# Kernel tuning notes

Measured on AMD Instinct MI355X. Metric: run time of the kernel, lower is better.

Reference implementation:

```python
import jax, jax.numpy as jnp
import numpy as np

B, N = 4, 4096
CIN, COUT = 64, 64
K, R, BOX = 3, 32, 4
MLP = COUT * 4
HEADS = 4
EPS = 0.0


def setup_inputs() -> dict:
    key = jax.random.key(0)
    ks = jax.random.split(key, 16)
    s = lambda i, shape: jax.random.normal(ks[i], shape, jnp.float32) * 0.05
    return dict(
        features=jax.random.normal(ks[0], (B, CIN, N), jnp.float32),
        coords=jax.random.normal(ks[1], (B, 3, N), jnp.float32),
        conv_w=s(2, (COUT, CIN, K, K, K)), conv_b=jnp.zeros((COUT,), jnp.float32),
        ln1_g=jnp.ones((COUT,), jnp.float32), ln1_b=jnp.zeros((COUT,), jnp.float32),
        qkv_w=s(3, (3 * COUT, COUT)), qkv_b=jnp.zeros((3 * COUT,), jnp.float32),
        proj_w=s(4, (COUT, COUT)), proj_b=jnp.zeros((COUT,), jnp.float32),
        ln2_g=jnp.ones((COUT,), jnp.float32), ln2_b=jnp.zeros((COUT,), jnp.float32),
        mlp_w1=s(5, (MLP, COUT)), mlp_b1=jnp.zeros((MLP,), jnp.float32),
        mlp_w2=s(6, (COUT, MLP)), mlp_b2=jnp.zeros((COUT,), jnp.float32),
        se_w1=s(7, (COUT // 8, COUT)), se_w2=s(8, (COUT, COUT // 8)),
        pt_in_w=s(9, (COUT, CIN)), pt_in_b=jnp.zeros((COUT,), jnp.float32),
        q_w=s(10, (COUT // 4, COUT)), k_w=s(11, (COUT // 4, COUT)),
        v_w=s(12, (COUT, COUT)),
        trans_w=s(13, (COUT, COUT)), trans_b=jnp.zeros((COUT,), jnp.float32),
    )


def layernorm(x, g, b):
    m = x.mean(-1, keepdims=True)
    v = x.var(-1, keepdims=True)
    return (x - m) * jax.lax.rsqrt(v + 1e-5) * g + b


def voxelize(features, coords):
    # PVCNN-style: center, normalize to [0,1], scale to [0, R-1]; scatter-mean.
    c = coords - coords.mean(axis=2, keepdims=True)  # (B,3,N)
    mx = jnp.sqrt((c ** 2).sum(axis=1, keepdims=True)).max(axis=2, keepdims=True)
    nc = c / (2.0 * mx + EPS) + 0.5
    nc = jnp.clip(nc * R, 0.0, R - 1)  # float coords in [0, R-1]
    vc = jnp.round(nc).astype(jnp.int32)
    idx = (vc[:, 0] * R + vc[:, 1]) * R + vc[:, 2]
    idx = (idx + jnp.arange(B, dtype=jnp.int32)[:, None] * R ** 3).reshape(-1)
    flat = features.transpose(0, 2, 1).reshape(B * N, CIN)
    sums = jax.ops.segment_sum(flat, idx, num_segments=B * R ** 3)
    cnt = jax.ops.segment_sum(jnp.ones((B * N,), jnp.float32), idx, num_segments=B * R ** 3)
    avg = sums / jnp.maximum(cnt, 1.0)[:, None]
    grid = avg.reshape(B, R, R, R, CIN).transpose(0, 4, 1, 2, 3)  # (B,C,R,R,R)
    return grid, nc


def devoxelize(grid, nc):
    # trilinear gather from (B,C,R,R,R) at float coords nc (B,3,N)
    g = grid.reshape(B, COUT, R ** 3)
    x0 = jnp.floor(nc)
    f = nc - x0
    x0 = x0.astype(jnp.int32)
    out = jnp.zeros((B, COUT, N), jnp.float32)
    for dx in (0, 1):
        for dy in (0, 1):
            for dz in (0, 1):
                xi = jnp.clip(x0[:, 0] + dx, 0, R - 1)
                yi = jnp.clip(x0[:, 1] + dy, 0, R - 1)
                zi = jnp.clip(x0[:, 2] + dz, 0, R - 1)
                idx = (xi * R + yi) * R + zi  # (B,N)
                w = ((f[:, 0] if dx else 1 - f[:, 0]) *
                     (f[:, 1] if dy else 1 - f[:, 1]) *
                     (f[:, 2] if dz else 1 - f[:, 2]))
                vals = jnp.take_along_axis(g, jnp.broadcast_to(idx[:, None, :], (B, COUT, N)), axis=2)
                out = out + vals * w[:, None, :]
    return out


def voxel_encoder(grid, conv_w, conv_b, ln1_g, ln1_b, qkv_w, qkv_b, proj_w, proj_b,
                  ln2_g, ln2_b, mlp_w1, mlp_b1, mlp_w2, mlp_b2):
    x = jax.lax.conv_general_dilated(grid, conv_w, (1, 1, 1), 'SAME',
                                     dimension_numbers=('NCDHW', 'OIDHW', 'NCDHW'))
    x = jax.nn.relu(x + conv_b[None, :, None, None, None])
    nb = R // BOX
    # window partition -> (B*nb^3, BOX^3, C)
    t = x.transpose(0, 2, 3, 4, 1).reshape(B, nb, BOX, nb, BOX, nb, BOX, COUT)
    t = t.transpose(0, 1, 3, 5, 2, 4, 6, 7).reshape(B * nb ** 3, BOX ** 3, COUT)
    h = layernorm(t, ln1_g, ln1_b)
    qkv = h @ qkv_w.T + qkv_b
    q, k, v = jnp.split(qkv, 3, axis=-1)
    hd = COUT // HEADS
    sh = lambda z: z.reshape(z.shape[0], z.shape[1], HEADS, hd).transpose(0, 2, 1, 3)
    q, k, v = sh(q), sh(k), sh(v)
    attn = jax.nn.softmax(jnp.einsum('whid,whjd->whij', q, k) / np.float32(np.sqrt(hd)), axis=-1)
    o = jnp.einsum('whij,whjd->whid', attn, v).transpose(0, 2, 1, 3).reshape(t.shape)
    t = t + (o @ proj_w.T + proj_b)
    h = layernorm(t, ln2_g, ln2_b)
    t = t + (jax.nn.gelu(h @ mlp_w1.T + mlp_b1) @ mlp_w2.T + mlp_b2)
    t = t.reshape(B, nb, nb, nb, BOX, BOX, BOX, COUT)
    t = t.transpose(0, 1, 4, 2, 5, 3, 6, 7).reshape(B, R, R, R, COUT)
    return t.transpose(0, 4, 1, 2, 3)


def se3d(x, w1, w2):
    s = x.mean(axis=(2, 3, 4))  # (B,C)
    s = jax.nn.sigmoid(jax.nn.relu(s @ w1.T) @ w2.T)
    return x * s[:, :, None, None, None]


def point_branch(features, pt_in_w, pt_in_b, q_w, k_w, v_w, trans_w, trans_b):
    # PCT-style offset self-attention over points (shared transformer)
    x = jax.nn.relu(jnp.einsum('oc,bcn->bon', pt_in_w, features) + pt_in_b[None, :, None])
    q = jnp.einsum('dc,bcn->bdn', q_w, x)
    k = jnp.einsum('dc,bcn->bdn', k_w, x)
    v = jnp.einsum('oc,bcn->bon', v_w, x)
    attn = jax.nn.softmax(jnp.einsum('bdn,bdm->bnm', q, k) / np.float32(np.sqrt(q.shape[1])), axis=-1)
    o = jnp.einsum('bom,bnm->bon', v, attn)
    off = jax.nn.relu(jnp.einsum('oc,bcn->bon', trans_w, x - o) + trans_b[None, :, None])
    return x + off


def reference(features, coords, conv_w, conv_b, ln1_g, ln1_b, qkv_w, qkv_b, proj_w, proj_b,
              ln2_g, ln2_b, mlp_w1, mlp_b1, mlp_w2, mlp_b2, se_w1, se_w2,
              pt_in_w, pt_in_b, q_w, k_w, v_w, trans_w, trans_b):
    grid, nc = voxelize(features, coords)
    vf = voxel_encoder(grid, conv_w, conv_b, ln1_g, ln1_b, qkv_w, qkv_b, proj_w, proj_b,
                       ln2_g, ln2_b, mlp_w1, mlp_b1, mlp_w2, mlp_b2)
    vf = se3d(vf, se_w1, se_w2)
    vf = devoxelize(vf, nc)
    fused = vf + point_branch(features, pt_in_w, pt_in_b, q_w, k_w, v_w, trans_w, trans_b)
    return fused, coords
```

## Files before the change

### kernel.cpp

```cpp
#include <hip/hip_runtime.h>

#define BN 4
#define NP 4096
#define RV 32
#define VX (RV*RV*RV)

typedef __attribute__((ext_vector_type(8))) short bf16x8;
typedef __attribute__((ext_vector_type(4))) float f32x4;

__device__ __forceinline__ float bf2f(unsigned short u){
  union{unsigned u;float f;}v; v.u=((unsigned)u)<<16; return v.f; }
__device__ __forceinline__ unsigned short f2bf(float f){
  union{float f;unsigned u;}v; v.f=f; unsigned r=v.u + 0x7fffu + ((v.u>>16)&1u);
  return (unsigned short)(r>>16); }
__device__ __forceinline__ float2 bfp2f2(unsigned p){
  union{unsigned u;float f;}a,b; a.u=p<<16; b.u=p&0xffff0000u;
  float2 r; r.x=a.f; r.y=b.f; return r; }
__device__ __forceinline__ unsigned pack2bf(float a, float b){
  return (unsigned)f2bf(a) | ((unsigned)f2bf(b) << 16); }

union ABu { uint4 u; bf16x8 v; };

__global__ void stats_kernel(const float* __restrict__ coords, float* __restrict__ stats)
{
  __shared__ float red[256];
  __shared__ float mean[3];
  const int b = blockIdx.x;
  const int tid = threadIdx.x;
  float s0=0.f,s1=0.f,s2=0.f;
  for (int n = tid; n < NP; n += 256) {
    s0 += coords[((size_t)(b*3)+0)*NP + n];
    s1 += coords[((size_t)(b*3)+1)*NP + n];
    s2 += coords[((size_t)(b*3)+2)*NP + n];
  }
  float sv[3] = {s0,s1,s2};
  for (int ax = 0; ax < 3; ax++) {
    __syncthreads();
    red[tid] = sv[ax];
    __syncthreads();
    for (int st = 128; st > 0; st >>= 1) {
      if (tid < st) red[tid] += red[tid + st];
      __syncthreads();
    }
    if (tid == 0) mean[ax] = red[0] * (1.f / NP);
  }
  __syncthreads();
  float mx = 0.f;
  for (int n = tid; n < NP; n += 256) {
    float d0 = coords[((size_t)(b*3)+0)*NP + n] - mean[0];
    float d1 = coords[((size_t)(b*3)+1)*NP + n] - mean[1];
    float d2 = coords[((size_t)(b*3)+2)*NP + n] - mean[2];
    mx = fmaxf(mx, sqrtf(d0*d0 + d1*d1 + d2*d2));
  }
  __syncthreads();
  red[tid] = mx;
  __syncthreads();
  for (int st = 128; st > 0; st >>= 1) {
    if (tid < st) red[tid] = fmaxf(red[tid], red[tid + st]);
    __syncthreads();
  }
  if (tid == 0) {
    stats[b*4+0] = mean[0]; stats[b*4+1] = mean[1];
    stats[b*4+2] = mean[2]; stats[b*4+3] = red[0];
  }
}

__global__ void scatter_kernel(const float* __restrict__ features,
                               const float* __restrict__ coords,
                               const float* __restrict__ stats,
                               float* __restrict__ nc,
                               float* __restrict__ sums, float* __restrict__ cnt)
{
  int t = blockIdx.x*256 + threadIdx.x;
  int part = t & 3;
  int p = t >> 2;
  int b = p >> 12;
  int n = p & 4095;
  float m0 = stats[b*4+0], m1 = stats[b*4+1], m2 = stats[b*4+2], mx = stats[b*4+3];
  float inv = 1.f / (2.f * mx);
  float c0 = (coords[((size_t)(b*3)+0)*NP + n] - m0) * inv + 0.5f;
  float c1 = (coords[((size_t)(b*3)+1)*NP + n] - m1) * inv + 0.5f;
  float c2 = (coords[((size_t)(b*3)+2)*NP + n] - m2) * inv + 0.5f;
  float g0 = fminf(fmaxf(c0 * 32.f, 0.f), 31.f);
  float g1 = fminf(fmaxf(c1 * 32.f, 0.f), 31.f);
  float g2 = fminf(fmaxf(c2 * 32.f, 0.f), 31.f);
  int v0 = (int)rintf(g0), v1 = (int)rintf(g1), v2 = (int)rintf(g2);
  int idx = (v0*32 + v1)*32 + v2 + b*VX;
  if (part == 0) {
    nc[((size_t)(b*3)+0)*NP + n] = g0;
    nc[((size_t)(b*3)+1)*NP + n] = g1;
    nc[((size_t)(b*3)+2)*NP + n] = g2;
    atomicAdd(&cnt[idx], 1.f);
  }
  const float* fp = features + (size_t)(b*64)*NP + n;
  float* sp = sums + (size_t)idx*64;
  for (int i = part*16; i < part*16+16; i++)
    atomicAdd(&sp[i], fp[(size_t)i*NP]);
}

__global__ void wprep_kernel(const float* __restrict__ wt, unsigned short* __restrict__ wpre)
{
  int t = blockIdx.x*256 + threadIdx.x;
  if (t >= 27*64*8) return;
  int c16 = t & 7, o = (t >> 3) & 63, tap = t >> 9;
  size_t dst = ((size_t)(tap*64 + o)*8 + (c16 ^ (o & 7))) * 8;
  #pragma unroll
  for (int j = 0; j < 8; j++) {
    int i = c16*8 + j;
    wpre[dst + j] = f2bf(wt[(o*64 + i)*27 + tap]);
  }
}

__global__ void eprep_kernel(const float* __restrict__ qkv_w, const float* __restrict__ proj_w,
                             const float* __restrict__ w1, const float* __restrict__ w2,
                             unsigned short* __restrict__ dst)
{
  int t = blockIdx.x*256 + threadIdx.x;
  float v;
  if (t < 12288)      v = qkv_w[t];
  else if (t < 16384) v = proj_w[t-12288];
  else if (t < 32768) v = w1[t-16384];
  else                v = w2[t-32768];
  dst[t] = f2bf(v);
}

__global__ __launch_bounds__(256) void conv_mfma_kernel(
    const float* __restrict__ sums, const float* __restrict__ cnt,
    const unsigned short* __restrict__ wpre,
    const float* __restrict__ bias, unsigned short* __restrict__ gout)
{
  __shared__ uint4 plane[6*34*8];
  __shared__ uint4 wsm[3*64*8];
  const int tid = threadIdx.x;
  const int blk = blockIdx.x;
  const int yq = blk & 7, z = (blk >> 3) & 31, b = blk >> 8;
  const int y0 = yq * 4;
  const int w  = tid >> 6;
  const int lm = tid & 15;
  const int kg = (tid >> 4) & 3;

  f32x4 acc[2][4];
  #pragma unroll
  for (int mt = 0; mt < 2; mt++)
    #pragma unroll
    for (int nt = 0; nt < 4; nt++)
      #pragma unroll
      for (int r = 0; r < 4; r++) acc[mt][nt][r] = 0.f;

  float bv[4];
  #pragma unroll
  for (int nt = 0; nt < 4; nt++) bv[nt] = bias[nt*16 + lm];

  for (int kd = 0; kd < 3; kd++) {
    const int zz = z + kd - 1;
    if (zz < 0 || zz >= 32) continue;
    __syncthreads();
    for (int e = tid; e < 6*34*8; e += 256) {
      int c16 = e & 7;
      int sx  = (e >> 3) % 34;
      int yl  = e / (34*8);
      int yy = y0 - 1 + yl, x = sx - 1;
      uint4 val = make_uint4(0u,0u,0u,0u);
      if (yy >= 0 && yy < 32 && x >= 0 && x < 32) {
        size_t vox = (size_t)(b*VX) + (zz*32 + yy)*32 + x;
        float rc = 1.f / fmaxf(cnt[vox], 1.f);
        const float* src = sums + vox*64 + c16*8;
        float4 f0 = *(const float4*)(src);
        float4 f1 = *(const float4*)(src + 4);
        val.x = pack2bf(f0.x*rc, f0.y*rc);
        val.y = pack2bf(f0.z*rc, f0.w*rc);
        val.z = pack2bf(f1.x*rc, f1.y*rc);
        val.w = pack2bf(f1.z*rc, f1.w*rc);
      }
      plane[(yl*34 + sx)*8 + (c16 ^ (sx & 7))] = val;
    }
    for (int kh = 0; kh < 3; kh++) {
      __syncthreads();
      const uint4* wsrc = (const uint4*)wpre + (size_t)((kd*3 + kh)*3)*512;
      for (int e = tid; e < 1536; e += 256) wsm[e] = wsrc[e];
      __syncthreads();
      const int yi = w + kh;
      #pragma unroll
      for (int kw = 0; kw < 3; kw++) {
        const int sxa = lm + kw, sxb = sxa + 16;
        const int swz = sxa & 7;
        #pragma unroll
        for (int ch = 0; ch < 2; ch++) {
          const int cb = ch*4 + kg;
          ABu a0, a1, w0, w1, w2, w3;
          a0.u = plane[(yi*34 + sxa)*8 + (cb ^ swz)];
          a1.u = plane[(yi*34 + sxb)*8 + (cb ^ swz)];
          const int wsz = cb ^ (lm & 7);
          w0.u = wsm[(kw*64 +      lm)*8 + wsz];
          w1.u = wsm[(kw*64 + 16 + lm)*8 + wsz];
          w2.u = wsm[(kw*64 + 32 + lm)*8 + wsz];
          w3.u = wsm[(kw*64 + 48 + lm)*8 + wsz];
          acc[0][0] = __builtin_amdgcn_mfma_f32_16x16x32_bf16(a0.v, w0.v, acc[0][0], 0,0,0);
          acc[1][0] = __builtin_amdgcn_mfma_f32_16x16x32_bf16(a1.v, w0.v, acc[1][0], 0,0,0);
          acc[0][1] = __builtin_amdgcn_mfma_f32_16x16x32_bf16(a0.v, w1.v, acc[0][1], 0,0,0);
          acc[1][1] = __builtin_amdgcn_mfma_f32_16x16x32_bf16(a1.v, w1.v, acc[1][1], 0,0,0);
          acc[0][2] = __builtin_amdgcn_mfma_f32_16x16x32_bf16(a0.v, w2.v, acc[0][2], 0,0,0);
          acc[1][2] = __builtin_amdgcn_mfma_f32_16x16x32_bf16(a1.v, w2.v, acc[1][2], 0,0,0);
          acc[0][3] = __builtin_amdgcn_mfma_f32_16x16x32_bf16(a0.v, w3.v, acc[0][3], 0,0,0);
          acc[1][3] = __builtin_amdgcn_mfma_f32_16x16x32_bf16(a1.v, w3.v, acc[1][3], 0,0,0);
        }
      }
    }
  }
  const int y = y0 + w;
  #pragma unroll
  for (int mt = 0; mt < 2; mt++) {
    #pragma unroll
    for (int r = 0; r < 4; r++) {
      const int x = mt*16 + kg*4 + r;
      unsigned short* dst = gout + ((size_t)(b*VX) + (z*32 + y)*32 + x)*64 + lm;
      #pragma unroll
      for (int nt = 0; nt < 4; nt++)
        dst[nt*16] = f2bf(fmaxf(acc[mt][nt][r] + bv[nt], 0.f));
    }
  }
}

__global__ __launch_bounds__(256) void encoder_kernel(
    unsigned short* __restrict__ grid,
    const float* __restrict__ ln1_g, const float* __restrict__ ln1_b,
    const float* __restrict__ qkv_b, const float* __restrict__ proj_b,
    const float* __restrict__ ln2_g, const float* __restrict__ ln2_b,
    const float* __restrict__ b1, const float* __restrict__ b2,
    const unsigned short* __restrict__ encw,
    float* __restrict__ se_sum)
{
  __shared__ unsigned short t_b[64*72];
  __shared__ unsigned short h_b[64*72];
  __shared__ unsigned short q_b[64*72];
  __shared__ unsigned short k_b[64*72];
  __shared__ unsigned short v_b[64*72];
  __shared__ float mean_s[64], rstd_s[64];
  __shared__ float sered[256];

  const unsigned short* wqb = encw;
  const unsigned short* wpb = encw + 12288;
  const unsigned short* w1b = encw + 16384;
  const unsigned short* w2b = encw + 32768;

  const int tid = threadIdx.x;
  const int w = tid >> 6;
  const int lane = tid & 63;
  const int cl = lane & 15;
  const int quad = lane >> 4;
  const int win = blockIdx.x;
  const int b = win >> 9, wn = win & 511;
  const int zb = wn >> 6, yb = (wn >> 3) & 7, xb = wn & 7;
  const size_t gb = (size_t)b * VX * 64;

  for (int e = tid; e < 1024; e += 256) {
    int tok = e >> 4, cg = e & 15;
    int zl = tok >> 4, yl = (tok >> 2) & 3, xl = tok & 3;
    int vox = ((zb*4+zl)*32 + (yb*4+yl))*32 + (xb*4+xl);
    *(uint2*)(t_b + tok*72 + cg*4) = *(const uint2*)(grid + gb + (size_t)vox*64 + cg*4);
  }
  __syncthreads();
  {
    int i = tid >> 2, part = tid & 3;
    float sum = 0.f, sq = 0.f;
    for (int c = part; c < 64; c += 4) { float x = bf2f(t_b[i*72+c]); sum += x; sq += x*x; }
    sum += __shfl_xor(sum, 1); sq += __shfl_xor(sq, 1);
    sum += __shfl_xor(sum, 2); sq += __shfl_xor(sq, 2);
    if (part == 0) {
      float m = sum * (1.f/64.f);
      float var = sq * (1.f/64.f) - m*m;
      mean_s[i] = m; rstd_s[i] = rsqrtf(var + 1e-5f);
    }
  }
  __syncthreads();
  for (int e = tid; e < 4096; e += 256) {
    int tok = e >> 6, c = e & 63;
    float h = (bf2f(t_b[tok*72+c]) - mean_s[tok]) * rstd_s[tok] * ln1_g[c] + ln1_b[c];
    h_b[tok*72 + c] = f2bf(h);
  }
  __syncthreads();
  {
    #pragma unroll
    for (int ci = 0; ci < 3; ci++) {
      const int d0 = 48*w + ci*16;
      ABu a0, a1;
      a0.u = *(const uint4*)(wqb + (d0 + cl)*64 + quad*8);
      a1.u = *(const uint4*)(wqb + (d0 + cl)*64 + 32 + quad*8);
      float4 bias4 = *(const float4*)(qkv_b + d0 + quad*4);
      #pragma unroll
      for (int tt = 0; tt < 4; tt++) {
        ABu h0, h1;
        h0.u = *(const uint4*)(h_b + (tt*16 + cl)*72 + quad*8);
        h1.u = *(const uint4*)(h_b + (tt*16 + cl)*72 + 32 + quad*8);
        f32x4 d = {0.f,0.f,0.f,0.f};
        d = __builtin_amdgcn_mfma_f32_16x16x32_bf16(a0.v, h0.v, d, 0,0,0);
        d = __builtin_amdgcn_mfma_f32_16x16x32_bf16(a1.v, h1.v, d, 0,0,0);
        if (d0 < 64) {
          *(uint2*)(q_b + (tt*16+cl)*72 + d0 + quad*4) =
            make_uint2(pack2bf((d[0]+bias4.x)*0.25f, (d[1]+bias4.y)*0.25f),
                       pack2bf((d[2]+bias4.z)*0.25f, (d[3]+bias4.w)*0.25f));
        } else if (d0 < 128) {
          *(uint2*)(k_b + (tt*16+cl)*72 + (d0-64) + quad*4) =
            make_uint2(pack2bf(d[0]+bias4.x, d[1]+bias4.y),
                       pack2bf(d[2]+bias4.z, d[3]+bias4.w));
        } else {
          const float* bp = (const float*)&bias4;
          #pragma unroll
          for (int r = 0; r < 4; r++)
            v_b[((d0-128) + quad*4 + r)*72 + tt*16 + cl] = f2bf(d[r] + bp[r]);
        }
      }
    }
  }
  __syncthreads();
  uint2 pk[4];
  {
    const uint4 z4 = make_uint4(0u,0u,0u,0u);
    #pragma unroll
    for (int h = 0; h < 4; h++) {
      const int hb = h*16;
      ABu bq;
      if (quad < 2) bq.u = *(const uint4*)(q_b + (w*16 + cl)*72 + hb + quad*8);
      else bq.u = z4;
      float sc[4][4];
      #pragma unroll
      for (int tj = 0; tj < 4; tj++) {
        ABu ak;
        if (quad < 2) ak.u = *(const uint4*)(k_b + (tj*16 + cl)*72 + hb + quad*8);
        else ak.u = z4;
        f32x4 d = {0.f,0.f,0.f,0.f};
        d = __builtin_amdgcn_mfma_f32_16x16x32_bf16(ak.v, bq.v, d, 0,0,0);
        #pragma unroll
        for (int r = 0; r < 4; r++) sc[tj][r] = d[r];
      }
      float mx = -1e30f;
      #pragma unroll
      for (int tj = 0; tj < 4; tj++)
        #pragma unroll
        for (int r = 0; r < 4; r++) mx = fmaxf(mx, sc[tj][r]);
      mx = fmaxf(mx, __shfl_xor(mx, 16));
      mx = fmaxf(mx, __shfl_xor(mx, 32));
      float psum = 0.f;
      #pragma unroll
      for (int tj = 0; tj < 4; tj++) {
        float p0 = __expf(sc[tj][0]-mx), p1 = __expf(sc[tj][1]-mx);
        float p2 = __expf(sc[tj][2]-mx), p3 = __expf(sc[tj][3]-mx);
        psum += p0+p1+p2+p3;
        *(uint2*)(h_b + (w*16+cl)*72 + tj*16 + quad*4) =
            make_uint2(pack2bf(p0,p1), pack2bf(p2,p3));
      }
      psum += __shfl_xor(psum, 16);
      psum += __shfl_xor(psum, 32);
      float inv = 1.f / psum;
      f32x4 oacc = {0.f,0.f,0.f,0.f};
      #pragma unroll
      for (int kk = 0; kk < 2; kk++) {
        ABu av, bp;
        av.u = *(const uint4*)(v_b + (hb + cl)*72 + kk*32 + quad*8);
        bp.u = *(const uint4*)(h_b + (w*16 + cl)*72 + kk*32 + quad*8);
        oacc = __builtin_amdgcn_mfma_f32_16x16x32_bf16(av.v, bp.v, oacc, 0,0,0);
      }
      pk[h] = make_uint2(pack2bf(oacc[0]*inv, oacc[1]*inv),
                         pack2bf(oacc[2]*inv, oacc[3]*inv));
    }
  }
  __syncthreads();
  #pragma unroll
  for (int h = 0; h < 4; h++)
    *(uint2*)(k_b + (w*16+cl)*72 + h*16 + quad*4) = pk[h];
  __syncthreads();
  {
    const int c0 = w*16;
    ABu a0, a1;
    a0.u = *(const uint4*)(wpb + (c0 + cl)*64 + quad*8);
    a1.u = *(const uint4*)(wpb + (c0 + cl)*64 + 32 + quad*8);
    float4 pb4 = *(const float4*)(proj_b + c0 + quad*4);
    #pragma unroll
    for (int tt = 0; tt < 4; tt++) {
      ABu o0, o1;
      o0.u = *(const uint4*)(k_b + (tt*16 + cl)*72 + quad*8);
      o1.u = *(const uint4*)(k_b + (tt*16 + cl)*72 + 32 + quad*8);
      f32x4 d = {0.f,0.f,0.f,0.f};
      d = __builtin_amdgcn_mfma_f32_16x16x32_bf16(a0.v, o0.v, d, 0,0,0);
      d = __builtin_amdgcn_mfma_f32_16x16x32_bf16(a1.v, o1.v, d, 0,0,0);
      uint2* tp = (uint2*)(t_b + (tt*16+cl)*72 + c0 + quad*4);
      uint2 told = *tp;
      float2 t01 = bfp2f2(told.x), t23 = bfp2f2(told.y);
      *tp = make_uint2(pack2bf(t01.x + d[0] + pb4.x, t01.y + d[1] + pb4.y),
                       pack2bf(t23.x + d[2] + pb4.z, t23.y + d[3] + pb4.w));
    }
  }
  __syncthreads();
  {
    int i = tid >> 2, part = tid & 3;
    float sum = 0.f, sq = 0.f;
    for (int c = part; c < 64; c += 4) { float x = bf2f(t_b[i*72+c]); sum += x; sq += x*x; }
    sum += __shfl_xor(sum, 1); sq += __shfl_xor(sq, 1);
    sum += __shfl_xor(sum, 2); sq += __shfl_xor(sq, 2);
    if (part == 0) {
      float m = sum * (1.f/64.f);
      float var = sq * (1.f/64.f) - m*m;
      mean_s[i] = m; rstd_s[i] = rsqrtf(var + 1e-5f);
    }
  }
  __syncthreads();
  for (int e = tid; e < 4096; e += 256) {
    int tok = e >> 6, c = e & 63;
    float h = (bf2f(t_b[tok*72+c]) - mean_s[tok]) * rstd_s[tok] * ln2_g[c] + ln2_b[c];
    h_b[tok*72 + c] = f2bf(h);
  }
  __syncthreads();
  {
    const int c0 = w*16;
    ABu hb0[4], hb1[4];
    #pragma unroll
    for (int tt = 0; tt < 4; tt++) {
      hb0[tt].u = *(const uint4*)(h_b + (tt*16 + cl)*72 + quad*8);
      hb1[tt].u = *(const uint4*)(h_b + (tt*16 + cl)*72 + 32 + quad*8);
    }
    f32x4 acc2[4];
    #pragma unroll
    for (int tt = 0; tt < 4; tt++)
      #pragma unroll
      for (int r = 0; r < 4; r++) acc2[tt][r] = 0.f;
    for (int ch = 0; ch < 4; ch++) {
      const int m0 = ch*64 + w*16;
      ABu a0, a1;
      a0.u = *(const uint4*)(w1b + (m0 + cl)*64 + quad*8);
      a1.u = *(const uint4*)(w1b + (m0 + cl)*64 + 32 + quad*8);
      float4 b14 = *(const float4*)(b1 + m0 + quad*4);
      const float* bp = (const float*)&b14;
      #pragma unroll
      for (int tt = 0; tt < 4; tt++) {
        f32x4 d = {0.f,0.f,0.f,0.f};
        d = __builtin_amdgcn_mfma_f32_16x16x32_bf16(a0.v, hb0[tt].v, d, 0,0,0);
        d = __builtin_amdgcn_mfma_f32_16x16x32_bf16(a1.v, hb1[tt].v, d, 0,0,0);
        float g[4];
        #pragma unroll
        for (int r = 0; r < 4; r++) {
          float x = d[r] + bp[r];
          float u = 1.5957691f * (x + 0.044715f*x*x*x);
          g[r] = x / (1.f + __expf(-u));
        }
        *(uint2*)(q_b + (tt*16+cl)*72 + w*16 + quad*4) =
            make_uint2(pack2bf(g[0],g[1]), pack2bf(g[2],g[3]));
      }
      __syncthreads();
      ABu a20, a21;
      a20.u = *(const uint4*)(w2b + (c0 + cl)*256 + ch*64 + quad*8);
      a21.u = *(const uint4*)(w2b + (c0 + cl)*256 + ch*64 + 32 + quad*8);
      #pragma unroll
      for (int tt = 0; tt < 4; tt++) {
        ABu bh0, bh1;
        bh0.u = *(const uint4*)(q_b + (tt*16 + cl)*72 + quad*8);
        bh1.u = *(const uint4*)(q_b + (tt*16 + cl)*72 + 32 + quad*8);
        acc2[tt] = __builtin_amdgcn_mfma_f32_16x16x32_bf16(a20.v, bh0.v, acc2[tt], 0,0,0);
        acc2[tt] = __builtin_amdgcn_mfma_f32_16x16x32_bf16(a21.v, bh1.v, acc2[tt], 0,0,0);
      }
      __syncthreads();
    }
    float4 b24 = *(const float4*)(b2 + c0 + quad*4);
    #pragma unroll
    for (int tt = 0; tt < 4; tt++) {
      uint2* tp = (uint2*)(t_b + (tt*16+cl)*72 + c0 + quad*4);
      uint2 told = *tp;
      float2 t01 = bfp2f2(told.x), t23 = bfp2f2(told.y);
      *tp = make_uint2(pack2bf(t01.x + acc2[tt][0] + b24.x, t01.y + acc2[tt][1] + b24.y),
                       pack2bf(t23.x + acc2[tt][2] + b24.z, t23.y + acc2[tt][3] + b24.w));
    }
  }
  __syncthreads();
  for (int e = tid; e < 1024; e += 256) {
    int tok = e >> 4, cg = e & 15;
    int zl = tok >> 4, yl = (tok >> 2) & 3, xl = tok & 3;
    int vox = ((zb*4+zl)*32 + (yb*4+yl))*32 + (xb*4+xl);
    *(uint2*)(grid + gb + (size_t)vox*64 + cg*4) = *(const uint2*)(t_b + tok*72 + cg*4);
  }
  {
    int c = tid & 63, quarter = tid >> 6;
    float ps = 0.f;
    #pragma unroll
    for (int t = 0; t < 16; t++) ps += bf2f(t_b[(quarter*16+t)*72 + c]);
    sered[quarter*64 + c] = ps;
  }
  __syncthreads();
  if (tid < 64)
    atomicAdd(&se_sum[b*64 + tid],
              sered[tid] + sered[64+tid] + sered[128+tid] + sered[192+tid]);
}

__global__ void se_kernel(const float* __restrict__ se_sum, const float* __restrict__ w1,
                          const float* __restrict__ w2, float* __restrict__ scale)
{
  __shared__ float mean_s[256];
  __shared__ float z1[32];
  int tid = threadIdx.x;
  mean_s[tid] = se_sum[tid] * (1.f / VX);
  __syncthreads();
  if (tid < 32) {
    int bb = tid >> 3, j = tid & 7;
    float a = 0.f;
    for (int c = 0; c < 64; c++) a += mean_s[bb*64 + c] * w1[j*64 + c];
    z1[tid] = fmaxf(a, 0.f);
  }
  __syncthreads();
  int b = tid >> 6, c = tid & 63;
  float a = 0.f;
  for (int j = 0; j < 8; j++) a += z1[b*8 + j] * w2[c*8 + j];
  scale[tid] = 1.f / (1.f + __expf(-a));
}

__global__ __launch_bounds__(256) void point_in_kernel(
    const float* __restrict__ features,
    const float* __restrict__ pt_in_w, const float* __restrict__ pt_in_b,
    const float* __restrict__ q_w, const float* __restrict__ k_w,
    const float* __restrict__ v_w,
    float* __restrict__ x_t, unsigned short* __restrict__ q_bf,
    unsigned short* __restrict__ k_bf, unsigned short* __restrict__ v_tt)
{
  __shared__ float f_s[64*65];
  __shared__ float x_s[64*65];
  const int tid = threadIdx.x;
  const int blk = blockIdx.x;
  const int b = blk >> 6;
  const int n0 = (blk & 63) * 64;
  for (int e = tid; e < 4096; e += 256) {
    int i = e >> 6, nl = e & 63;
    f_s[nl*65 + i] = features[((size_t)(b*64 + i))*NP + n0 + nl];
  }
  __syncthreads();
  const int c = tid & 63, g = tid >> 6;
  const int t0 = g * 16;
  {
    float acc[16];
    #pragma unroll
    for (int t = 0; t < 16; t++) acc[t] = 0.f;
    for (int i = 0; i < 64; i++) {
      float wv = pt_in_w[c*64 + i];
      #pragma unroll
      for (int t = 0; t < 16; t++) acc[t] += f_s[(t0+t)*65 + i] * wv;
    }
    float bb = pt_in_b[c];
    #pragma unroll
    for (int t = 0; t < 16; t++) {
      float x = fmaxf(acc[t] + bb, 0.f);
      x_s[(t0+t)*65 + c] = x;
      x_t[((size_t)(b*NP) + n0 + t0 + t)*64 + c] = x;
    }
  }
  __syncthreads();
  {
    float acc[16];
    #pragma unroll
    for (int t = 0; t < 16; t++) acc[t] = 0.f;
    for (int k = 0; k < 64; k++) {
      float wv = v_w[c*64 + k];
      #pragma unroll
      for (int t = 0; t < 16; t++) acc[t] += x_s[(t0+t)*65 + k] * wv;
    }
    #pragma unroll
    for (int t = 0; t < 16; t++)
      v_tt[((size_t)(b*64) + c)*NP + n0 + t0 + t] = f2bf(acc[t]);
  }
  if (tid < 128) {
    int d = tid & 15, which = (tid >> 4) & 1, g2 = tid >> 5;
    int t0b = g2 * 16;
    const float* wp = which ? k_w : q_w;
    float scl = which ? 1.f : 0.25f;
    float acc[16];
    #pragma unroll
    for (int t = 0; t < 16; t++) acc[t] = 0.f;
    for (int cc = 0; cc < 64; cc++) {
      float wv = wp[d*64 + cc];
      #pragma unroll
      for (int t = 0; t < 16; t++) acc[t] += x_s[(t0b+t)*65 + cc] * wv;
    }
    unsigned short* dst = which ? k_bf : q_bf;
    #pragma unroll
    for (int t = 0; t < 16; t++)
      dst[((size_t)(b*NP) + n0 + t0b + t)*16 + d] = f2bf(acc[t] * scl);
  }
}

__global__ __launch_bounds__(256) void point_attn_kernel(
    const unsigned short* __restrict__ q_bf, const unsigned short* __restrict__ k_bf,
    const unsigned short* __restrict__ v_tt,
    float* __restrict__ opart, float2* __restrict__ mlbuf)
{
  __shared__ unsigned short q_s[64*24];
  __shared__ unsigned short k_sh[2][64*24];
  __shared__ unsigned short v_sh[2][64*72];
  __shared__ unsigned short p_s[64*72];
  const int tid = threadIdx.x;
  const int blk = blockIdx.x;
  const int b = blk >> 8;
  const int nb = (blk >> 2) & 63;
  const int s = blk & 3;
  const int n0 = nb * 64;
  const int t_beg = s*16, t_end = s*16 + 16;
  const int w = tid >> 6;
  const int lane = tid & 63;
  const int cl = lane & 15;
  const int quad = lane >> 4;
  const uint4 z4 = make_uint4(0u,0u,0u,0u);

  const unsigned* qbu = (const unsigned*)q_bf;
  const unsigned* kbu = (const unsigned*)k_bf;
  const unsigned* vtu = (const unsigned*)v_tt;
  unsigned* q_su = (unsigned*)q_s;

  {
    unsigned* kd = (unsigned*)k_sh[0];
    unsigned* vd = (unsigned*)v_sh[0];
    for (int e = tid; e < 512; e += 256) {
      int tok = e >> 3, du = e & 7;
      q_su[tok*12 + du] = qbu[((size_t)(b*NP) + n0 + tok)*8 + du];
      kd[tok*12 + du]   = kbu[((size_t)(b*NP) + t_beg*64 + tok)*8 + du];
    }
    for (int e = tid; e < 2048; e += 256) {
      int cc = e >> 5, tu = e & 31;
      vd[cc*36 + tu] = vtu[((size_t)(b*64) + cc)*2048 + t_beg*32 + tu];
    }
  }
  float m_run = -1e30f, l_run = 0.f;
  f32x4 acc[4];
  #pragma unroll
  for (int ct = 0; ct < 4; ct++)
    #pragma unroll
    for (int r = 0; r < 4; r++) acc[ct][r] = 0.f;
  __syncthreads();

  ABu bq;
  if (quad < 2) bq.u = *(const uint4*)(q_s + (w*16 + cl)*24 + quad*8);
  else bq.u = z4;

  for (int t = t_beg; t < t_end; t++) {
    const int cur = t & 1;
    unsigned pk[2], pv[8];
    if (t+1 < t_end) {
      const int m1 = (t+1)*64;
      #pragma unroll
      for (int i = 0; i < 2; i++) {
        int e = tid + i*256;
        pk[i] = kbu[((size_t)(b*NP) + m1 + (e>>3))*8 + (e&7)];
      }
      #pragma unroll
      for (int i = 0; i < 8; i++) {
        int e = tid + i*256;
        pv[i] = vtu[((size_t)(b*64) + (e>>5))*2048 + (m1>>1) + (e&31)];
      }
    }
    const unsigned short* ks = k_sh[cur];
    const unsigned short* vs = v_sh[cur];
    float sc[4][4];
    #pragma unroll
    for (int tj = 0; tj < 4; tj++) {
      ABu ak;
      if (quad < 2) ak.u = *(const uint4*)(ks + (tj*16 + cl)*24 + quad*8);
      else ak.u = z4;
      f32x4 d = {0.f,0.f,0.f,0.f};
      d = __builtin_amdgcn_mfma_f32_16x16x32_bf16(ak.v, bq.v, d, 0,0,0);
      #pragma unroll
      for (int r = 0; r < 4; r++) sc[tj][r] = d[r];
    }
    float tmax = -1e30f;
    #pragma unroll
    for (int tj = 0; tj < 4; tj++)
      #pragma unroll
      for (int r = 0; r < 4; r++) tmax = fmaxf(tmax, sc[tj][r]);
    tmax = fmaxf(tmax, __shfl_xor(tmax, 16));
    tmax = fmaxf(tmax, __shfl_xor(tmax, 32));
    float mnew = fmaxf(m_run, tmax);
    float alpha = __expf(m_run - mnew);
    float psum = 0.f;
    #pragma unroll
    for (int tj = 0; tj < 4; tj++) {
      float p0 = __expf(sc[tj][0]-mnew), p1 = __expf(sc[tj][1]-mnew);
      float p2 = __expf(sc[tj][2]-mnew), p3 = __expf(sc[tj][3]-mnew);
      psum += p0+p1+p2+p3;
      *(uint2*)(p_s + (w*16+cl)*72 + tj*16 + quad*4) =
          make_uint2(pack2bf(p0,p1), pack2bf(p2,p3));
    }
    psum += __shfl_xor(psum, 16);
    psum += __shfl_xor(psum, 32);
    l_run = l_run*alpha + psum;
    m_run = mnew;
    #pragma unroll
    for (int ct = 0; ct < 4; ct++)
      #pragma unroll
      for (int r = 0; r < 4; r++) acc[ct][r] *= alpha;
    #pragma unroll
    for (int kk = 0; kk < 2; kk++) {
      ABu bp;
      bp.u = *(const uint4*)(p_s + (w*16 + cl)*72 + kk*32 + quad*8);
      #pragma unroll
      for (int ct = 0; ct < 4; ct++) {
        ABu av;
        av.u = *(const uint4*)(vs + (ct*16 + cl)*72 + kk*32 + quad*8);
        acc[ct] = __builtin_amdgcn_mfma_f32_16x16x32_bf16(av.v, bp.v, acc[ct], 0,0,0);
      }
    }
    __syncthreads();
    if (t+1 < t_end) {
      unsigned* kd = (unsigned*)k_sh[1-cur];
      unsigned* vd = (unsigned*)v_sh[1-cur];
      #pragma unroll
      for (int i = 0; i < 2; i++) {
        int e = tid + i*256;
        kd[(e>>3)*12 + (e&7)] = pk[i];
      }
      #pragma unroll
      for (int i = 0; i < 8; i++) {
        int e = tid + i*256;
        vd[(e>>5)*36 + (e&31)] = pv[i];
      }
    }
    __syncthreads();
  }
  const int tok = n0 + w*16 + cl;
  #pragma unroll
  for (int ct = 0; ct < 4; ct++) {
    float4 o4;
    o4.x = acc[ct][0]; o4.y = acc[ct][1]; o4.z = acc[ct][2]; o4.w = acc[ct][3];
    *(float4*)&opart[(((size_t)(s*BN + b))*NP + tok)*64 + ct*16 + quad*4] = o4;
  }
  if (quad == 0)
    mlbuf[(size_t)(s*BN + b)*NP + tok] = make_float2(m_run, l_run);
}

__global__ __launch_bounds__(256) void fuse_kernel(
    const float* __restrict__ x_t, const float* __restrict__ opart,
    const float2* __restrict__ mlbuf,
    const float* __restrict__ trans_w, const float* __restrict__ trans_b,
    const unsigned short* __restrict__ grid, const float* __restrict__ se_scale,
    const float* __restrict__ nc, float* __restrict__ out)
{
  __shared__ float tw_s[64*65];
  __shared__ float d_s[32*65];
  __shared__ float r_s[64*33];
  __shared__ float mw[32][6];
  const int tid = threadIdx.x;
  const int blk = blockIdx.x;
  const int b = blk >> 7;
  const int n0 = (blk & 127) * 32;
  for (int e = tid; e < 4096; e += 256) {
    int c = e >> 6, k = e & 63;
    tw_s[c*65 + k] = trans_w[e];
  }
  if (tid < 32) {
    int nl = tid;
    float m[4], l[4];
    #pragma unroll
    for (int s = 0; s < 4; s++) {
      float2 v = mlbuf[(size_t)(s*BN + b)*NP + n0 + nl];
      m[s] = v.x; l[s] = v.y;
    }
    float M = fmaxf(fmaxf(m[0], m[1]), fmaxf(m[2], m[3]));
    float L = 0.f;
    #pragma unroll
    for (int s = 0; s < 4; s++) {
      float ws = __expf(m[s] - M);
      mw[nl][s] = ws;
      L += l[s] * ws;
    }
    mw[nl][4] = 1.f / L;
  }
  __syncthreads();
  for (int e = tid; e < 2048; e += 256) {
    int nl = e >> 6, c = e & 63;
    size_t pbase = ((size_t)(b*NP) + n0 + nl)*64 + c;
    const size_t sstr = (size_t)BN*NP*64;
    float o = opart[pbase]        * mw[nl][0] + opart[pbase +   sstr] * mw[nl][1]
            + opart[pbase+2*sstr] * mw[nl][2] + opart[pbase + 3*sstr] * mw[nl][3];
    o *= mw[nl][4];
    d_s[nl*65 + c] = x_t[pbase] - o;
  }
  __syncthreads();
  const int cl = tid & 63, g = tid >> 6;
  const float ses = se_scale[b*64 + cl];
  const float tb = trans_b[cl];
  for (int t = 0; t < 8; t++) {
    int nl = g*8 + t;
    int n = n0 + nl;
    float off = 0.f;
    for (int k = 0; k < 64; k++) off += tw_s[cl*65 + k] * d_s[nl*65 + k];
    off = fmaxf(off + tb, 0.f);
    float ncx = nc[((size_t)(b*3)+0)*NP + n];
    float ncy = nc[((size_t)(b*3)+1)*NP + n];
    float ncz = nc[((size_t)(b*3)+2)*NP + n];
    float fx0 = floorf(ncx), fy0 = floorf(ncy), fz0 = floorf(ncz);
    int x0 = (int)fx0, y0 = (int)fy0, z0 = (int)fz0;
    float fx = ncx - fx0, fy = ncy - fy0, fz = ncz - fz0;
    float wx[2] = {1.f-fx, fx}, wy[2] = {1.f-fy, fy}, wz[2] = {1.f-fz, fz};
    float vf = 0.f;
    #pragma unroll
    for (int cor = 0; cor < 8; cor++) {
      int dx = cor >> 2, dy = (cor >> 1) & 1, dz = cor & 1;
      int xi = min(x0+dx, 31), yi = min(y0+dy, 31), zi = min(z0+dz, 31);
      float wgt = wx[dx]*wy[dy]*wz[dz];
      vf += wgt * bf2f(grid[((size_t)(b*VX) + (xi*32+yi)*32 + zi)*64 + cl]);
    }
    vf *= ses;
    float xval = x_t[((size_t)(b*NP) + n)*64 + cl];
    r_s[cl*33 + nl] = xval + off + vf;
  }
  __syncthreads();
  for (int e = tid; e < 2048; e += 256) {
    int c = e >> 5, nl = e & 31;
    out[((size_t)(b*64) + c)*NP + n0 + nl] = r_s[c*33 + nl];
  }
}

extern "C" void kernel_launch(void* const* d_in, const int* in_sizes, int n_in,
                              void* d_out, int out_size, void* d_ws, size_t ws_size,
                              hipStream_t stream)
{
  const float* features = (const float*)d_in[0];
  const float* coords   = (const float*)d_in[1];
  const float* conv_w   = (const float*)d_in[2];
  const float* conv_b   = (const float*)d_in[3];
  const float* ln1_g    = (const float*)d_in[4];
  const float* ln1_b    = (const float*)d_in[5];
  const float* qkv_w    = (const float*)d_in[6];
  const float* qkv_b    = (const float*)d_in[7];
  const float* proj_w   = (const float*)d_in[8];
  const float* proj_b   = (const float*)d_in[9];
  const float* ln2_g    = (const float*)d_in[10];
  const float* ln2_b    = (const float*)d_in[11];
  const float* mlp_w1   = (const float*)d_in[12];
  const float* mlp_b1   = (const float*)d_in[13];
  const float* mlp_w2   = (const float*)d_in[14];
  const float* mlp_b2   = (const float*)d_in[15];
  const float* se_w1    = (const float*)d_in[16];
  const float* se_w2    = (const float*)d_in[17];
  const float* pt_in_w  = (const float*)d_in[18];
  const float* pt_in_b  = (const float*)d_in[19];
  const float* q_w      = (const float*)d_in[20];
  const float* k_w      = (const float*)d_in[21];
  const float* v_w      = (const float*)d_in[22];
  const float* v_trans_w= (const float*)d_in[23];
  const float* v_trans_b= (const float*)d_in[24];

  char* ws = (char*)d_ws;
  float* stats    = (float*)(ws + 0);
  float* se_sum   = (float*)(ws + 256);
  float* se_scale = (float*)(ws + 1280);
  float* nc       = (float*)(ws + 4096);
  float* cnt      = (float*)(ws + 200704);
  float* grid0    = (float*)(ws + 724992);
  unsigned short* grid1b = (unsigned short*)(ws + 34279424);
  float* x_t = (float*)(ws + 724992);
  unsigned short* q_bf = (unsigned short*)(ws + 724992 + 4194304);
  unsigned short* k_bf = (unsigned short*)(ws + 724992 + 5242880);
  unsigned short* v_tt = (unsigned short*)(ws + 724992 + 6291456);
  float*  opart = (float*)(ws + 724992 + 10485760);
  float2* mlbuf = (float2*)(ws + 724992 + 27787264);
  unsigned short* wpre = (unsigned short*)d_out;
  unsigned short* encw = (unsigned short*)((char*)d_out + 221184);

  hipMemsetAsync(se_sum, 0, 1024, stream);
  hipMemsetAsync(cnt, 0, 524288 + 33554432, stream);

  wprep_kernel<<<54, 256, 0, stream>>>(conv_w, wpre);
  eprep_kernel<<<192, 256, 0, stream>>>(qkv_w, proj_w, mlp_w1, mlp_w2, encw);
  stats_kernel<<<BN, 256, 0, stream>>>(coords, stats);
  scatter_kernel<<<256, 256, 0, stream>>>(features, coords, stats, nc, grid0, cnt);
  conv_mfma_kernel<<<1024, 256, 0, stream>>>(grid0, cnt, wpre, conv_b, grid1b);
  encoder_kernel<<<2048, 256, 0, stream>>>(grid1b, ln1_g, ln1_b, qkv_b, proj_b,
      ln2_g, ln2_b, mlp_b1, mlp_b2, encw, se_sum);
  se_kernel<<<1, 256, 0, stream>>>(se_sum, se_w1, se_w2, se_scale);
  point_in_kernel<<<256, 256, 0, stream>>>(features, pt_in_w, pt_in_b, q_w, k_w, v_w,
      x_t, q_bf, k_bf, v_tt);
  point_attn_kernel<<<1024, 256, 0, stream>>>(q_bf, k_bf, v_tt, opart, mlbuf);
  fuse_kernel<<<512, 256, 0, stream>>>(x_t, opart, mlbuf, v_trans_w, v_trans_b,
      grid1b, se_scale, nc, (float*)d_out);
  hipMemcpyAsync((char*)d_out + (size_t)BN*64*NP*4, coords, (size_t)BN*3*NP*4,
                 hipMemcpyDeviceToDevice, stream);
}
```

Measured before the change: 428.7 us.

## Move point input projections to bf16 MFMA and vectorize encoder layernorms

Rewrites point_in_kernel so the pt_in, v, q and k projections run as bf16 MFMA tiles instead of scalar fp32 FMA loops. The weights are pre-converted in eprep, with the q scale folded into the weights and the bias. In the encoder, grid load/store and the layernorm passes are vectorized, and LN2 statistics are fused into the projection epilogue via shuffles. The SE partial sums are also reorganized. The cost is lower precision, since features and x are now rounded to bf16 before the matmuls.

```diff
diff --git a/kernel.cpp b/kernel.cpp
--- a/kernel.cpp
+++ b/kernel.cpp
@@ -113,14 +113,25 @@
 
 __global__ void eprep_kernel(const float* __restrict__ qkv_w, const float* __restrict__ proj_w,
                              const float* __restrict__ w1, const float* __restrict__ w2,
+                             const float* __restrict__ pt_in_w, const float* __restrict__ q_w,
+                             const float* __restrict__ k_w, const float* __restrict__ v_w,
                              unsigned short* __restrict__ dst)
 {
   int t = blockIdx.x*256 + threadIdx.x;
+  if (t >= 59392) return;
   float v;
-  if (t < 12288)      v = qkv_w[t];
+  if (t < 4096)       v = qkv_w[t] * 0.25f;
+  else if (t < 12288) v = qkv_w[t];
   else if (t < 16384) v = proj_w[t-12288];
   else if (t < 32768) v = w1[t-16384];
-  else                v = w2[t-32768];
+  else if (t < 49152) v = w2[t-32768];
+  else {
+    int t2 = t - 49152;
+    if (t2 < 4096)      v = pt_in_w[t2];
+    else if (t2 < 5120) v = q_w[t2-4096] * 0.25f;
+    else if (t2 < 6144) v = k_w[t2-5120];
+    else                v = v_w[t2-6144];
+  }
   dst[t] = f2bf(v);
 }
 
@@ -236,7 +247,7 @@
   __shared__ unsigned short k_b[64*72];
   __shared__ unsigned short v_b[64*72];
   __shared__ float mean_s[64], rstd_s[64];
-  __shared__ float sered[256];
+  __shared__ float scratch[1024];
 
   const unsigned short* wqb = encw;
   const unsigned short* wpb = encw + 12288;
@@ -253,17 +264,27 @@
   const int zb = wn >> 6, yb = (wn >> 3) & 7, xb = wn & 7;
   const size_t gb = (size_t)b * VX * 64;
 
-  for (int e = tid; e < 1024; e += 256) {
-    int tok = e >> 4, cg = e & 15;
+  for (int e = tid; e < 512; e += 256) {
+    int tok = e >> 3, cg8 = e & 7;
     int zl = tok >> 4, yl = (tok >> 2) & 3, xl = tok & 3;
     int vox = ((zb*4+zl)*32 + (yb*4+yl))*32 + (xb*4+xl);
-    *(uint2*)(t_b + tok*72 + cg*4) = *(const uint2*)(grid + gb + (size_t)vox*64 + cg*4);
+    *(uint4*)(t_b + tok*72 + cg8*8) = *(const uint4*)(grid + gb + (size_t)vox*64 + cg8*8);
   }
   __syncthreads();
   {
     int i = tid >> 2, part = tid & 3;
+    ABu r0, r1;
+    r0.u = *(const uint4*)(t_b + i*72 + part*16);
+    r1.u = *(const uint4*)(t_b + i*72 + part*16 + 8);
     float sum = 0.f, sq = 0.f;
-    for (int c = part; c < 64; c += 4) { float x = bf2f(t_b[i*72+c]); sum += x; sq += x*x; }
+    const unsigned* u0 = (const unsigned*)&r0;
+    const unsigned* u1 = (const unsigned*)&r1;
+    #pragma unroll
+    for (int j = 0; j < 4; j++) {
+      float2 a = bfp2f2(u0[j]); float2 c = bfp2f2(u1[j]);
+      sum += a.x + a.y + c.x + c.y;
+      sq  += a.x*a.x + a.y*a.y + c.x*c.x + c.y*c.y;
+    }
     sum += __shfl_xor(sum, 1); sq += __shfl_xor(sq, 1);
     sum += __shfl_xor(sum, 2); sq += __shfl_xor(sq, 2);
     if (part == 0) {
@@ -273,10 +294,22 @@
     }
   }
   __syncthreads();
-  for (int e = tid; e < 4096; e += 256) {
-    int tok = e >> 6, c = e & 63;
-    float h = (bf2f(t_b[tok*72+c]) - mean_s[tok]) * rstd_s[tok] * ln1_g[c] + ln1_b[c];
-    h_b[tok*72 + c] = f2bf(h);
+  {
+    const int cg = tid & 15, tq = tid >> 4;
+    float4 g4 = *(const float4*)(ln1_g + cg*4);
+    float4 b4 = *(const float4*)(ln1_b + cg*4);
+    #pragma unroll
+    for (int k = 0; k < 4; k++) {
+      int tok = tq + k*16;
+      uint2 tv = *(const uint2*)(t_b + tok*72 + cg*4);
+      float2 x01 = bfp2f2(tv.x), x23 = bfp2f2(tv.y);
+      float m = mean_s[tok], r = rstd_s[tok];
+      float h0 = (x01.x-m)*r*g4.x + b4.x;
+      float h1 = (x01.y-m)*r*g4.y + b4.y;
+      float h2 = (x23.x-m)*r*g4.z + b4.z;
+      float h3 = (x23.y-m)*r*g4.w + b4.w;
+      *(uint2*)(h_b + tok*72 + cg*4) = make_uint2(pack2bf(h0,h1), pack2bf(h2,h3));
+    }
   }
   __syncthreads();
   {
@@ -287,6 +320,7 @@
       a0.u = *(const uint4*)(wqb + (d0 + cl)*64 + quad*8);
       a1.u = *(const uint4*)(wqb + (d0 + cl)*64 + 32 + quad*8);
       float4 bias4 = *(const float4*)(qkv_b + d0 + quad*4);
+      if (d0 < 64) { bias4.x *= 0.25f; bias4.y *= 0.25f; bias4.z *= 0.25f; bias4.w *= 0.25f; }
       #pragma unroll
       for (int tt = 0; tt < 4; tt++) {
         ABu h0, h1;
@@ -297,8 +331,8 @@
         d = __builtin_amdgcn_mfma_f32_16x16x32_bf16(a1.v, h1.v, d, 0,0,0);
         if (d0 < 64) {
           *(uint2*)(q_b + (tt*16+cl)*72 + d0 + quad*4) =
-            make_uint2(pack2bf((d[0]+bias4.x)*0.25f, (d[1]+bias4.y)*0.25f),
-                       pack2bf((d[2]+bias4.z)*0.25f, (d[3]+bias4.w)*0.25f));
+            make_uint2(pack2bf(d[0]+bias4.x, d[1]+bias4.y),
+                       pack2bf(d[2]+bias4.z, d[3]+bias4.w));
         } else if (d0 < 128) {
           *(uint2*)(k_b + (tt*16+cl)*72 + (d0-64) + quad*4) =
             make_uint2(pack2bf(d[0]+bias4.x, d[1]+bias4.y),
@@ -386,28 +420,47 @@
       uint2* tp = (uint2*)(t_b + (tt*16+cl)*72 + c0 + quad*4);
       uint2 told = *tp;
       float2 t01 = bfp2f2(told.x), t23 = bfp2f2(told.y);
-      *tp = make_uint2(pack2bf(t01.x + d[0] + pb4.x, t01.y + d[1] + pb4.y),
-                       pack2bf(t23.x + d[2] + pb4.z, t23.y + d[3] + pb4.w));
-    }
-  }
-  __syncthreads();
-  {
-    int i = tid >> 2, part = tid & 3;
-    float sum = 0.f, sq = 0.f;
-    for (int c = part; c < 64; c += 4) { float x = bf2f(t_b[i*72+c]); sum += x; sq += x*x; }
-    sum += __shfl_xor(sum, 1); sq += __shfl_xor(sq, 1);
-    sum += __shfl_xor(sum, 2); sq += __shfl_xor(sq, 2);
-    if (part == 0) {
-      float m = sum * (1.f/64.f);
-      float var = sq * (1.f/64.f) - m*m;
-      mean_s[i] = m; rstd_s[i] = rsqrtf(var + 1e-5f);
-    }
-  }
-  __syncthreads();
-  for (int e = tid; e < 4096; e += 256) {
-    int tok = e >> 6, c = e & 63;
-    float h = (bf2f(t_b[tok*72+c]) - mean_s[tok]) * rstd_s[tok] * ln2_g[c] + ln2_b[c];
-    h_b[tok*72 + c] = f2bf(h);
+      float n0v = t01.x + d[0] + pb4.x;
+      float n1v = t01.y + d[1] + pb4.y;
+      float n2v = t23.x + d[2] + pb4.z;
+      float n3v = t23.y + d[3] + pb4.w;
+      *tp = make_uint2(pack2bf(n0v,n1v), pack2bf(n2v,n3v));
+      float s = n0v+n1v+n2v+n3v;
+      float qq = n0v*n0v + n1v*n1v + n2v*n2v + n3v*n3v;
+      s  += __shfl_xor(s, 16);  s  += __shfl_xor(s, 32);
+      qq += __shfl_xor(qq, 16); qq += __shfl_xor(qq, 32);
+      if (quad == 0) {
+        scratch[(tt*16+cl)*4 + w] = s;
+        scratch[256 + (tt*16+cl)*4 + w] = qq;
+      }
+    }
+  }
+  __syncthreads();
+  if (tid < 64) {
+    float s  = scratch[tid*4] + scratch[tid*4+1] + scratch[tid*4+2] + scratch[tid*4+3];
+    float qq = scratch[256+tid*4] + scratch[256+tid*4+1]
+             + scratch[256+tid*4+2] + scratch[256+tid*4+3];
+    float m = s * (1.f/64.f);
+    float var = qq * (1.f/64.f) - m*m;
+    mean_s[tid] = m; rstd_s[tid] = rsqrtf(var + 1e-5f);
+  }
+  __syncthreads();
+  {
+    const int cg = tid & 15, tq = tid >> 4;
+    float4 g4 = *(const float4*)(ln2_g + cg*4);
+    float4 b4 = *(const float4*)(ln2_b + cg*4);
+    #pragma unroll
+    for (int k = 0; k < 4; k++) {
+      int tok = tq + k*16;
+      uint2 tv = *(const uint2*)(t_b + tok*72 + cg*4);
+      float2 x01 = bfp2f2(tv.x), x23 = bfp2f2(tv.y);
+      float m = mean_s[tok], r = rstd_s[tok];
+      float h0 = (x01.x-m)*r*g4.x + b4.x;
+      float h1 = (x01.y-m)*r*g4.y + b4.y;
+      float h2 = (x23.x-m)*r*g4.z + b4.z;
+      float h3 = (x23.y-m)*r*g4.w + b4.w;
+      *(uint2*)(h_b + tok*72 + cg*4) = make_uint2(pack2bf(h0,h1), pack2bf(h2,h3));
+    }
   }
   __syncthreads();
   {
@@ -470,23 +523,32 @@
     }
   }
   __syncthreads();
-  for (int e = tid; e < 1024; e += 256) {
-    int tok = e >> 4, cg = e & 15;
+  for (int e = tid; e < 512; e += 256) {
+    int tok = e >> 3, cg8 = e & 7;
     int zl = tok >> 4, yl = (tok >> 2) & 3, xl = tok & 3;
     int vox = ((zb*4+zl)*32 + (yb*4+yl))*32 + (xb*4+xl);
-    *(uint2*)(grid + gb + (size_t)vox*64 + cg*4) = *(const uint2*)(t_b + tok*72 + cg*4);
-  }
-  {
-    int c = tid & 63, quarter = tid >> 6;
-    float ps = 0.f;
-    #pragma unroll
-    for (int t = 0; t < 16; t++) ps += bf2f(t_b[(quarter*16+t)*72 + c]);
-    sered[quarter*64 + c] = ps;
-  }
-  __syncthreads();
-  if (tid < 64)
-    atomicAdd(&se_sum[b*64 + tid],
-              sered[tid] + sered[64+tid] + sered[128+tid] + sered[192+tid]);
+    *(uint4*)(grid + gb + (size_t)vox*64 + cg8*8) = *(const uint4*)(t_b + tok*72 + cg8*8);
+  }
+  {
+    const int cg = tid & 15, tq = tid >> 4;
+    float4 p = {0.f,0.f,0.f,0.f};
+    #pragma unroll
+    for (int k = 0; k < 4; k++) {
+      int tok = tq + k*16;
+      uint2 tv = *(const uint2*)(t_b + tok*72 + cg*4);
+      float2 x01 = bfp2f2(tv.x), x23 = bfp2f2(tv.y);
+      p.x += x01.x; p.y += x01.y; p.z += x23.x; p.w += x23.y;
+    }
+    ((float4*)scratch)[cg*16 + tq] = p;
+  }
+  __syncthreads();
+  if (tid < 64) {
+    int cg = tid >> 2, j = tid & 3;
+    float s = 0.f;
+    #pragma unroll
+    for (int g = 0; g < 16; g++) s += scratch[(cg*16+g)*4 + j];
+    atomicAdd(&se_sum[b*64 + tid], s);
+  }
 }
 
 __global__ void se_kernel(const float* __restrict__ se_sum, const float* __restrict__ w1,
@@ -511,74 +573,89 @@
 }
 
 __global__ __launch_bounds__(256) void point_in_kernel(
-    const float* __restrict__ features,
-    const float* __restrict__ pt_in_w, const float* __restrict__ pt_in_b,
-    const float* __restrict__ q_w, const float* __restrict__ k_w,
-    const float* __restrict__ v_w,
+    const float* __restrict__ features, const float* __restrict__ pt_in_b,
+    const unsigned short* __restrict__ ptw,
     float* __restrict__ x_t, unsigned short* __restrict__ q_bf,
     unsigned short* __restrict__ k_bf, unsigned short* __restrict__ v_tt)
 {
-  __shared__ float f_s[64*65];
-  __shared__ float x_s[64*65];
+  __shared__ unsigned short f_b[64*72];
+  __shared__ unsigned short x_b[64*72];
   const int tid = threadIdx.x;
   const int blk = blockIdx.x;
   const int b = blk >> 6;
   const int n0 = (blk & 63) * 64;
+  const int w = tid >> 6;
+  const int lane = tid & 63;
+  const int cl = lane & 15;
+  const int quad = lane >> 4;
+
   for (int e = tid; e < 4096; e += 256) {
-    int i = e >> 6, nl = e & 63;
-    f_s[nl*65 + i] = features[((size_t)(b*64 + i))*NP + n0 + nl];
-  }
-  __syncthreads();
-  const int c = tid & 63, g = tid >> 6;
-  const int t0 = g * 16;
-  {
-    float acc[16];
-    #pragma unroll
-    for (int t = 0; t < 16; t++) acc[t] = 0.f;
-    for (int i = 0; i < 64; i++) {
-      float wv = pt_in_w[c*64 + i];
-      #pragma unroll
-      for (int t = 0; t < 16; t++) acc[t] += f_s[(t0+t)*65 + i] * wv;
-    }
-    float bb = pt_in_b[c];
-    #pragma unroll
-    for (int t = 0; t < 16; t++) {
-      float x = fmaxf(acc[t] + bb, 0.f);
-      x_s[(t0+t)*65 + c] = x;
-      x_t[((size_t)(b*NP) + n0 + t0 + t)*64 + c] = x;
-    }
-  }
-  __syncthreads();
-  {
-    float acc[16];
-    #pragma unroll
-    for (int t = 0; t < 16; t++) acc[t] = 0.f;
-    for (int k = 0; k < 64; k++) {
-      float wv = v_w[c*64 + k];
-      #pragma unroll
-      for (int t = 0; t < 16; t++) acc[t] += x_s[(t0+t)*65 + k] * wv;
-    }
-    #pragma unroll
-    for (int t = 0; t < 16; t++)
-      v_tt[((size_t)(b*64) + c)*NP + n0 + t0 + t] = f2bf(acc[t]);
-  }
-  if (tid < 128) {
-    int d = tid & 15, which = (tid >> 4) & 1, g2 = tid >> 5;
-    int t0b = g2 * 16;
-    const float* wp = which ? k_w : q_w;
-    float scl = which ? 1.f : 0.25f;
-    float acc[16];
-    #pragma unroll
-    for (int t = 0; t < 16; t++) acc[t] = 0.f;
-    for (int cc = 0; cc < 64; cc++) {
-      float wv = wp[d*64 + cc];
-      #pragma unroll
-      for (int t = 0; t < 16; t++) acc[t] += x_s[(t0b+t)*65 + cc] * wv;
-    }
+    int c = e >> 6, nl = e & 63;
+    f_b[nl*72 + c] = f2bf(features[((size_t)(b*64 + c))*NP + n0 + nl]);
+  }
+  __syncthreads();
+  const int m0 = w*16;
+  {
+    ABu a0, a1;
+    a0.u = *(const uint4*)(ptw + (m0 + cl)*64 + quad*8);
+    a1.u = *(const uint4*)(ptw + (m0 + cl)*64 + 32 + quad*8);
+    float4 bi = *(const float4*)(pt_in_b + m0 + quad*4);
+    #pragma unroll
+    for (int tt = 0; tt < 4; tt++) {
+      ABu f0, f1;
+      f0.u = *(const uint4*)(f_b + (tt*16 + cl)*72 + quad*8);
+      f1.u = *(const uint4*)(f_b + (tt*16 + cl)*72 + 32 + quad*8);
+      f32x4 d = {0.f,0.f,0.f,0.f};
+      d = __builtin_amdgcn_mfma_f32_16x16x32_bf16(a0.v, f0.v, d, 0,0,0);
+      d = __builtin_amdgcn_mfma_f32_16x16x32_bf16(a1.v, f1.v, d, 0,0,0);
+      float x0 = fmaxf(d[0]+bi.x, 0.f), x1 = fmaxf(d[1]+bi.y, 0.f);
+      float x2 = fmaxf(d[2]+bi.z, 0.f), x3 = fmaxf(d[3]+bi.w, 0.f);
+      const int n = tt*16 + cl;
+      *(float4*)&x_t[((size_t)(b*NP) + n0 + n)*64 + m0 + quad*4] =
+          make_float4(x0, x1, x2, x3);
+      *(uint2*)(x_b + n*72 + m0 + quad*4) = make_uint2(pack2bf(x0,x1), pack2bf(x2,x3));
+    }
+  }
+  __syncthreads();
+  {
+    const unsigned short* vwb = ptw + 6144;
+    ABu a0, a1;
+    a0.u = *(const uint4*)(vwb + (m0 + cl)*64 + quad*8);
+    a1.u = *(const uint4*)(vwb + (m0 + cl)*64 + 32 + quad*8);
+    #pragma unroll
+    for (int tt = 0; tt < 4; tt++) {
+      ABu x0, x1;
+      x0.u = *(const uint4*)(x_b + (tt*16 + cl)*72 + quad*8);
+      x1.u = *(const uint4*)(x_b + (tt*16 + cl)*72 + 32 + quad*8);
+      f32x4 d = {0.f,0.f,0.f,0.f};
+      d = __builtin_amdgcn_mfma_f32_16x16x32_bf16(a0.v, x0.v, d, 0,0,0);
+      d = __builtin_amdgcn_mfma_f32_16x16x32_bf16(a1.v, x1.v, d, 0,0,0);
+      const int n = n0 + tt*16 + cl;
+      #pragma unroll
+      for (int r = 0; r < 4; r++)
+        v_tt[((size_t)(b*64) + m0 + quad*4 + r)*NP + n] = f2bf(d[r]);
+    }
+  }
+  {
+    const int which = w & 1, half = w >> 1;
+    const unsigned short* wp = ptw + (which ? 5120 : 4096);
     unsigned short* dst = which ? k_bf : q_bf;
-    #pragma unroll
-    for (int t = 0; t < 16; t++)
-      dst[((size_t)(b*NP) + n0 + t0b + t)*16 + d] = f2bf(acc[t] * scl);
+    ABu a0, a1;
+    a0.u = *(const uint4*)(wp + cl*64 + quad*8);
+    a1.u = *(const uint4*)(wp + cl*64 + 32 + quad*8);
+    #pragma unroll
+    for (int th = 0; th < 2; th++) {
+      const int tt = half*2 + th;
+      ABu x0, x1;
+      x0.u = *(const uint4*)(x_b + (tt*16 + cl)*72 + quad*8);
+      x1.u = *(const uint4*)(x_b + (tt*16 + cl)*72 + 32 + quad*8);
+      f32x4 d = {0.f,0.f,0.f,0.f};
+      d = __builtin_amdgcn_mfma_f32_16x16x32_bf16(a0.v, x0.v, d, 0,0,0);
+      d = __builtin_amdgcn_mfma_f32_16x16x32_bf16(a1.v, x1.v, d, 0,0,0);
+      const int n = tt*16 + cl;
+      *(uint2*)(dst + ((size_t)(b*NP) + n0 + n)*16 + quad*4) =
+          make_uint2(pack2bf(d[0],d[1]), pack2bf(d[2],d[3]));
+    }
   }
 }
 
@@ -862,14 +939,15 @@
   hipMemsetAsync(cnt, 0, 524288 + 33554432, stream);
 
   wprep_kernel<<<54, 256, 0, stream>>>(conv_w, wpre);
-  eprep_kernel<<<192, 256, 0, stream>>>(qkv_w, proj_w, mlp_w1, mlp_w2, encw);
+  eprep_kernel<<<232, 256, 0, stream>>>(qkv_w, proj_w, mlp_w1, mlp_w2,
+      pt_in_w, q_w, k_w, v_w, encw);
   stats_kernel<<<BN, 256, 0, stream>>>(coords, stats);
   scatter_kernel<<<256, 256, 0, stream>>>(features, coords, stats, nc, grid0, cnt);
   conv_mfma_kernel<<<1024, 256, 0, stream>>>(grid0, cnt, wpre, conv_b, grid1b);
   encoder_kernel<<<2048, 256, 0, stream>>>(grid1b, ln1_g, ln1_b, qkv_b, proj_b,
       ln2_g, ln2_b, mlp_b1, mlp_b2, encw, se_sum);
   se_kernel<<<1, 256, 0, stream>>>(se_sum, se_w1, se_w2, se_scale);
-  point_in_kernel<<<256, 256, 0, stream>>>(features, pt_in_w, pt_in_b, q_w, k_w, v_w,
+  point_in_kernel<<<256, 256, 0, stream>>>(features, pt_in_b, encw + 49152,
       x_t, q_bf, k_bf, v_tt);
   point_attn_kernel<<<1024, 256, 0, stream>>>(q_bf, k_bf, v_tt, opart, mlbuf);
   fuse_kernel<<<512, 256, 0, stream>>>(x_t, opart, mlbuf, v_trans_w, v_trans_b,
```

New measurement: 398.3 us. 7.1% less time.
